# Performance work log

Hardware: AMD Instinct MI355X
Metric: run time of the kernel (lower is better)

The kernel has to match this reference:

```python
import jax, jax.numpy as jnp
import numpy as np
from jax import lax

# dims (see shape_source)
V, E = 100000, 200        # vocab, embedding dim
HID = 256; H = HID // 2    # BiLSTM hidden, per-direction
K = 24                     # tagset size (incl START/STOP)
B, T = 64, 1024
START, STOP = 0, 1
NEG = -10000.0


def setup_inputs() -> dict:
    key = jax.random.key(0)
    ks = jax.random.split(key, 16)
    s = 0.1  # init scale to keep LSTM gates in a sane range
    return {
        "sentences": jax.random.randint(ks[0], (B, T), 0, V, dtype=jnp.int32),
        "lens": jnp.full((B,), T, dtype=jnp.int32),
        "emb": jax.random.normal(ks[1], (V, E), dtype=jnp.float32) * s,
        # PyTorch LSTM layout: W_ih [4H, in], W_hh [4H, H], gate order i,f,g,o
        "W_ih_f": jax.random.normal(ks[2], (4 * H, E)) * s,
        "W_hh_f": jax.random.normal(ks[3], (4 * H, H)) * s,
        "b_ih_f": jax.random.normal(ks[4], (4 * H,)) * s,
        "b_hh_f": jax.random.normal(ks[5], (4 * H,)) * s,
        "W_ih_b": jax.random.normal(ks[6], (4 * H, E)) * s,
        "W_hh_b": jax.random.normal(ks[7], (4 * H, H)) * s,
        "b_ih_b": jax.random.normal(ks[8], (4 * H,)) * s,
        "b_hh_b": jax.random.normal(ks[9], (4 * H,)) * s,
        # init_hidden(): random h0/c0, [2 directions, B, H]
        "h0": jax.random.normal(ks[10], (2, B, H)),
        "c0": jax.random.normal(ks[11], (2, B, H)),
        # hidden2tag: nn.Linear(hidden_dim, K) -> weight [K, HID]
        "W_out": jax.random.normal(ks[12], (K, HID)) * s,
        "b_out": jax.random.normal(ks[13], (K,)) * s,
        "transitions": jax.random.normal(ks[14], (K, K)),  # [to, from]
    }


def _lstm_dir(x, W_ih, W_hh, b_ih, b_hh, h0, c0):
    """x: [T, B, in] -> hs: [T, B, H]. PyTorch LSTM cell math."""
    def step(carry, xt):
        h, c = carry
        g = xt @ W_ih.T + b_ih + h @ W_hh.T + b_hh  # [B, 4H]
        i, f, gg, o = jnp.split(g, 4, axis=-1)
        i = jax.nn.sigmoid(i); f = jax.nn.sigmoid(f)
        gg = jnp.tanh(gg); o = jax.nn.sigmoid(o)
        c = f * c + i * gg
        h = o * jnp.tanh(c)
        return (h, c), h
    _, hs = lax.scan(step, (h0, c0), x)
    return hs


def _viterbi_batch(feats, transitions):
    """feats: [B, T, K]. Batched version of _viterbi_decode.
    Returns (path_score [B], best_path [B, T])."""
    b = feats.shape[0]
    v0 = jnp.full((b, K), NEG, feats.dtype).at[:, START].set(0.0)
    transT = transitions.T  # [prev, next]

    def step(v, feat_t):
        # scores[b, prev, next] = v[b, prev] + trans(next <- prev)
        scores = v[:, :, None] + transT[None, :, :]
        best = jnp.max(scores, axis=1)          # [B, K]
        bptr = jnp.argmax(scores, axis=1)       # [B, K] best prev per next
        return best + feat_t, bptr

    v, bptrs = lax.scan(step, v0, jnp.swapaxes(feats, 0, 1))  # bptrs [T, B, K]
    terminal = v + transitions[STOP][None, :]
    path_score = jnp.max(terminal, axis=1)      # [B]
    last_tag = jnp.argmax(terminal, axis=1)     # [B]

    def back(tag, bp):
        prev = jnp.take_along_axis(bp, tag[:, None], axis=1)[:, 0]
        return prev, tag

    _, path = lax.scan(back, last_tag, bptrs, reverse=True)  # [T, B]
    return path_score, path.T


def reference(sentences, lens, emb, W_ih_f, W_hh_f, b_ih_f, b_hh_f,
              W_ih_b, W_hh_b, b_ih_b, b_hh_b, h0, c0, W_out, b_out,
              transitions):
    # embedding lookup; forward() packs raw w_embeds (dropout branch unused)
    x = emb[sentences]                       # [B, T, E]
    x = jnp.swapaxes(x, 0, 1)                # [T, B, E] (time-major like LSTM)
    hf = _lstm_dir(x, W_ih_f, W_hh_f, b_ih_f, b_hh_f, h0[0], c0[0])
    hb = _lstm_dir(x[::-1], W_ih_b, W_hh_b, b_ih_b, b_hh_b, h0[1], c0[1])[::-1]
    out = jnp.concatenate([hf, hb], axis=-1)  # [T, B, HID]
    feats = out @ W_out.T + b_out             # [T, B, K]
    feats = jnp.swapaxes(feats, 0, 1)          # [B, T, K]
    # all lens == T, so per-sentence slicing is the full sequence
    path_score, tag_seqs = _viterbi_batch(feats, transitions)
    return path_score, tag_seqs
```

## Files before the change

### kernel.cpp

```cpp
#include <hip/hip_runtime.h>
#include <math.h>

#define Ee   200
#define Hh   128
#define G4   512
#define Kk   24
#define Bb   64
#define Tt   1024
#define HIDd 256
#define NEGf (-10000.0f)
#define PSTR 9

__global__ __launch_bounds__(256) void k_wt(const float* __restrict__ Wf,
                                            const float* __restrict__ Wb,
                                            float* __restrict__ Wt) {
    int idx = blockIdx.x * 256 + threadIdx.x;
    if (idx >= Ee * 1024) return;
    int k = idx >> 10, n = idx & 1023;
    Wt[idx] = (n < G4) ? Wf[n * Ee + k] : Wb[(n - G4) * Ee + k];
}

__global__ __launch_bounds__(256, 2) void k_gemm2(const int* __restrict__ sent,
                                                  const float* __restrict__ emb,
                                                  const float* __restrict__ Wt,
                                                  float* __restrict__ Uc,
                                                  int c0T, int CT, int unified) {
    __shared__ float As[8][128];
    __shared__ float Bs[8][256];
    __shared__ int   toks[128];

    int tid = threadIdx.x;
    int n0  = blockIdx.x * 256;
    int m0  = blockIdx.y * 128;
    int dz  = blockIdx.z;
    int ty  = tid >> 4, tx = tid & 15;

    if (tid < 128) {
        int m = m0 + tid;
        int it = m >> 6, b = m & 63;
        int t = unified ? it : (dz ? (Tt - 1 - (c0T + it)) : (c0T + it));
        toks[tid] = sent[b * Tt + t];
    }
    __syncthreads();

    int am = tid & 127, ak4 = tid >> 7;
    int brow = tid >> 5, bc4 = tid & 31;

    const float* aptr = emb + (size_t)toks[am] * Ee + ak4 * 4;
    int bcol0 = (unified ? 0 : dz * G4) + n0;
    const float* bptr = Wt + (size_t)brow * 1024 + bcol0 + bc4 * 4;

    float acc[8][16];
#pragma unroll
    for (int i = 0; i < 8; ++i)
#pragma unroll
        for (int j = 0; j < 16; ++j) acc[i][j] = 0.f;

    float4 av  = *(const float4*)(aptr);
    float4 bv0 = *(const float4*)(bptr);
    float4 bv1 = *(const float4*)(bptr + 128);

    for (int kc = 0; kc < Ee; kc += 8) {
        As[ak4 * 4 + 0][am] = av.x;
        As[ak4 * 4 + 1][am] = av.y;
        As[ak4 * 4 + 2][am] = av.z;
        As[ak4 * 4 + 3][am] = av.w;
        *(float4*)&Bs[brow][bc4 * 4]       = bv0;
        *(float4*)&Bs[brow][128 + bc4 * 4] = bv1;
        __syncthreads();

        if (kc + 8 < Ee) {
            av  = *(const float4*)(aptr + kc + 8);
            bv0 = *(const float4*)(bptr + (size_t)(kc + 8) * 1024);
            bv1 = *(const float4*)(bptr + (size_t)(kc + 8) * 1024 + 128);
        }

#pragma unroll
        for (int k = 0; k < 8; ++k) {
            float a_[8], b_[16];
            *(float4*)&a_[0] = *(const float4*)&As[k][ty * 8];
            *(float4*)&a_[4] = *(const float4*)&As[k][ty * 8 + 4];
#pragma unroll
            for (int q = 0; q < 4; ++q)
                *(float4*)&b_[4 * q] = *(const float4*)&Bs[k][tx * 4 + 64 * q];
#pragma unroll
            for (int i = 0; i < 8; ++i)
#pragma unroll
                for (int j = 0; j < 16; ++j)
                    acc[i][j] = fmaf(a_[i], b_[j], acc[i][j]);
        }
        __syncthreads();
    }

    int dd   = unified ? (n0 >> 9) : dz;
    int ncol = unified ? (n0 & 511) : n0;
    float* base = Uc + (size_t)dd * ((size_t)CT * Bb * G4);
#pragma unroll
    for (int i = 0; i < 8; ++i) {
        float* dst = base + (size_t)(m0 + ty * 8 + i) * G4 + ncol + tx * 4;
#pragma unroll
        for (int q = 0; q < 4; ++q)
            *(float4*)(dst + 64 * q) = make_float4(acc[i][4 * q], acc[i][4 * q + 1],
                                                   acc[i][4 * q + 2], acc[i][4 * q + 3]);
    }
}

__global__ __launch_bounds__(512, 2) void k_lstm2(const float* __restrict__ Uc,
                                                  const float* __restrict__ Whh_f,
                                                  const float* __restrict__ Whh_b,
                                                  const float* __restrict__ bih_f,
                                                  const float* __restrict__ bhh_f,
                                                  const float* __restrict__ bih_b,
                                                  const float* __restrict__ bhh_b,
                                                  const float* __restrict__ h0v,
                                                  const float* __restrict__ c0v,
                                                  const float* __restrict__ Wout,
                                                  float* __restrict__ hst,
                                                  float* __restrict__ cst,
                                                  float* __restrict__ pf,
                                                  int c0T, int CT, int first, int unified) {
    __shared__ float hsh[Hh];
    __shared__ float gsh[G4];
    __shared__ float ps[(G4 + Kk) * PSTR];

    int tid  = threadIdx.x;
    int lane = tid & 63, wv = tid >> 6;
    int b = blockIdx.x & 63, d = blockIdx.x >> 6;

    const float* Whh = d ? Whh_b : Whh_f;
    float bias = d ? (bih_b[tid] + bhh_b[tid]) : (bih_f[tid] + bhh_f[tid]);

    float w[8][16];
#pragma unroll
    for (int ri = 0; ri < 8; ++ri) {
        const float* wr = Whh + (size_t)(ri * 64 + lane) * Hh + wv * 16;
#pragma unroll
        for (int c4 = 0; c4 < 4; ++c4)
            *(float4*)&w[ri][c4 * 4] = *(const float4*)(wr + c4 * 4);
    }
    float wt[16];
    if (lane < Kk) {
        const float* wr = Wout + (size_t)lane * HIDd + d * Hh + wv * 16;
#pragma unroll
        for (int c4 = 0; c4 < 4; ++c4)
            *(float4*)&wt[c4 * 4] = *(const float4*)(wr + c4 * 4);
    }

    float cc = 0.f;
    if (tid < Hh) {
        int si = (d * Bb + b) * Hh + tid;
        hsh[tid] = first ? h0v[si] : hst[si];
        cc       = first ? c0v[si] : cst[si];
    }
    __syncthreads();

    const float* Ub = Uc + (size_t)d * ((size_t)CT * Bb * G4);
    int u0 = unified ? (d ? (Tt - 1) : 0) : 0;
    int us = unified ? (d ? -1 : 1) : 1;

    float ucur = Ub[(size_t)u0 * (Bb * G4) + b * G4 + tid];
    float unext = 0.f;

    for (int i = 0; i <= CT; ++i) {
        int last = (i == CT);
        float hv[16];
        *(float4*)&hv[0]  = *(const float4*)&hsh[wv * 16];
        *(float4*)&hv[4]  = *(const float4*)&hsh[wv * 16 + 4];
        *(float4*)&hv[8]  = *(const float4*)&hsh[wv * 16 + 8];
        *(float4*)&hv[12] = *(const float4*)&hsh[wv * 16 + 12];

        if (lane < Kk) {
            float s = 0.f;
#pragma unroll
            for (int c = 0; c < 16; ++c) s = fmaf(wt[c], hv[c], s);
            ps[(G4 + lane) * PSTR + wv] = s;
        }
        if (!last) {
#pragma unroll
            for (int ri = 0; ri < 8; ++ri) {
                float s = 0.f;
#pragma unroll
                for (int c = 0; c < 16; ++c) s = fmaf(w[ri][c], hv[c], s);
                ps[(ri * 64 + lane) * PSTR + wv] = s;
            }
            if (i + 1 < CT)
                unext = Ub[(size_t)(u0 + (i + 1) * us) * (Bb * G4) + b * G4 + tid];
        }
        __syncthreads();

        if (!last) {
            const float* pr = ps + (size_t)tid * PSTR;
            float s = ((pr[0] + pr[1]) + (pr[2] + pr[3])) +
                      ((pr[4] + pr[5]) + (pr[6] + pr[7]));
            s += ucur + bias;
            int gt = tid >> 7;
            gsh[tid] = (gt == 2) ? tanhf(s) : 1.f / (1.f + expf(-s));
        }
        __syncthreads();

        if (!last && tid < Hh) {
            float gi = gsh[tid], gf = gsh[Hh + tid];
            float gg = gsh[2 * Hh + tid], go = gsh[3 * Hh + tid];
            cc = gf * cc + gi * gg;
            hsh[tid] = go * tanhf(cc);
        }
        if (tid >= 128 && tid < 128 + Kk && i >= 1) {
            int k = tid - 128;
            const float* pr = ps + (size_t)(G4 + k) * PSTR;
            float s = ((pr[0] + pr[1]) + (pr[2] + pr[3])) +
                      ((pr[4] + pr[5]) + (pr[6] + pr[7]));
            int tp = c0T + i - 1;
            int tg = d ? (Tt - 1 - tp) : tp;
            pf[((size_t)(d * Bb + b) * Tt + tg) * Kk + k] = s;
        }
        __syncthreads();
        ucur = unext;
    }

    if (tid < Hh) {
        int si = (d * Bb + b) * Hh + tid;
        hst[si] = hsh[tid];
        cst[si] = cc;
    }
}

#define CMB(av, ai, bv_, bi_, ov, oi)                         \
    { bool g = (bv_) > (av); ov = g ? (bv_) : (av); oi = g ? (bi_) : (ai); }

__global__ __launch_bounds__(64) void k_viterbi(const float* __restrict__ pf,
                                                const float* __restrict__ bout,
                                                const float* __restrict__ trans,
                                                float* __restrict__ out) {
    __shared__ unsigned char bptr[Tt * Kk];
    __shared__ float fsh[2][64][25];
    __shared__ float tsh[Kk];
    __shared__ unsigned char path[Tt];

    int lane = threadIdx.x;
    int b    = blockIdx.x;
    int half   = (lane >= Kk) ? 1 : 0;
    int n      = half ? (lane - Kk) : lane;
    int active = (lane < 2 * Kk);

    float tr[12];
    float bo = 0.f;
    if (active) {
#pragma unroll
        for (int j = 0; j < 12; ++j) tr[j] = trans[n * Kk + half * 12 + j];
        bo = bout[n];
    }
    float v = (lane == 0) ? 0.f : NEGf;

    const float* p0 = pf + (size_t)b * Tt * Kk;
    const float* p1 = pf + (size_t)(Bb + b) * Tt * Kk;

    float4 r0[6], r1[6];
#pragma unroll
    for (int j = 0; j < 6; ++j) {
        int f = 4 * (lane + 64 * j);
        r0[j] = *(const float4*)(p0 + f);
        r1[j] = *(const float4*)(p1 + f);
    }
#pragma unroll
    for (int j = 0; j < 6; ++j) {
        int f = 4 * (lane + 64 * j);
        int s = f / 24, k = f - 24 * s;
        fsh[0][s][k + 0] = r0[j].x + r1[j].x;
        fsh[0][s][k + 1] = r0[j].y + r1[j].y;
        fsh[0][s][k + 2] = r0[j].z + r1[j].z;
        fsh[0][s][k + 3] = r0[j].w + r1[j].w;
    }

    for (int c = 0; c < 16; ++c) {
        int cur = c & 1;
        if (c + 1 < 16) {
            const float* q0 = p0 + (c + 1) * 1536;
            const float* q1 = p1 + (c + 1) * 1536;
#pragma unroll
            for (int j = 0; j < 6; ++j) {
                int f = 4 * (lane + 64 * j);
                r0[j] = *(const float4*)(q0 + f);
                r1[j] = *(const float4*)(q1 + f);
            }
        }

        for (int s = 0; s < 64; ++s) {
            int t = c * 64 + s;
            if (active) {
                int pb = half * 12;
                float sc[12];
#pragma unroll
                for (int j = 0; j < 12; ++j) sc[j] = __shfl(v, pb + j) + tr[j];

                float l1v[6]; int l1i[6];
#pragma unroll
                for (int j = 0; j < 6; ++j)
                    CMB(sc[2 * j], 2 * j, sc[2 * j + 1], 2 * j + 1, l1v[j], l1i[j]);
                float l2v[3]; int l2i[3];
#pragma unroll
                for (int j = 0; j < 3; ++j)
                    CMB(l1v[2 * j], l1i[2 * j], l1v[2 * j + 1], l1i[2 * j + 1],
                        l2v[j], l2i[j]);
                float dv; int di;
                CMB(l2v[0], l2i[0], l2v[1], l2i[1], dv, di);
                float best; int bp;
                CMB(dv, di, l2v[2], l2i[2], best, bp);
                bp += pb;

                float ob  = __shfl(best, n + Kk);
                int   obp = __shfl(bp,   n + Kk);
                if (half == 0) {
                    if (ob > best) { best = ob; bp = obp; }
                    v = best + fsh[cur][s][n] + bo;
                    bptr[t * Kk + n] = (unsigned char)bp;
                }
            }
        }

        if (c + 1 < 16) {
#pragma unroll
            for (int j = 0; j < 6; ++j) {
                int f = 4 * (lane + 64 * j);
                int s = f / 24, k = f - 24 * s;
                fsh[cur ^ 1][s][k + 0] = r0[j].x + r1[j].x;
                fsh[cur ^ 1][s][k + 1] = r0[j].y + r1[j].y;
                fsh[cur ^ 1][s][k + 2] = r0[j].z + r1[j].z;
                fsh[cur ^ 1][s][k + 3] = r0[j].w + r1[j].w;
            }
        }
    }

    if (half == 0 && lane < Kk) tsh[n] = v + trans[1 * Kk + n];
    __syncthreads();

    if (lane == 0) {
        float bestv = tsh[0];
        int tag = 0;
        for (int q = 1; q < Kk; ++q)
            if (tsh[q] > bestv) { bestv = tsh[q]; tag = q; }
        out[b] = bestv;
        for (int t = Tt - 1; t >= 1; --t) {
            path[t] = (unsigned char)tag;
            tag = bptr[t * Kk + tag];
        }
        path[0] = (unsigned char)tag;
    }
    __syncthreads();

    float* otag = out + Bb + (size_t)b * Tt;
    for (int t = lane; t < Tt; t += 64) otag[t] = (float)path[t];
}

extern "C" void kernel_launch(void* const* d_in, const int* in_sizes, int n_in,
                              void* d_out, int out_size, void* d_ws, size_t ws_size,
                              hipStream_t stream) {
    const int*   sent  = (const int*)d_in[0];
    const float* emb   = (const float*)d_in[2];
    const float* Wih_f = (const float*)d_in[3];
    const float* Whh_f = (const float*)d_in[4];
    const float* bih_f = (const float*)d_in[5];
    const float* bhh_f = (const float*)d_in[6];
    const float* Wih_b = (const float*)d_in[7];
    const float* Whh_b = (const float*)d_in[8];
    const float* bih_b = (const float*)d_in[9];
    const float* bhh_b = (const float*)d_in[10];
    const float* h0    = (const float*)d_in[11];
    const float* c0    = (const float*)d_in[12];
    const float* Wout  = (const float*)d_in[13];
    const float* bout  = (const float*)d_in[14];
    const float* trans = (const float*)d_in[15];

    float* ws  = (float*)d_ws;
    float* Wt  = ws;
    float* pf  = Wt + 204800;
    float* hst = pf + 3145728;
    float* cst = hst + 16384;
    float* Uc  = cst + 16384;

    const size_t fixedf = 204800 + 3145728 + 16384 + 16384;
    size_t needU = (size_t)2 * Tt * Bb * G4;
    int unified = ((fixedf + needU) * 4 <= ws_size);

    k_wt<<<(Ee * 1024 + 255) / 256, 256, 0, stream>>>(Wih_f, Wih_b, Wt);

    if (unified) {
        k_gemm2<<<dim3(4, 512, 1), 256, 0, stream>>>(sent, emb, Wt, Uc, 0, Tt, 1);
        k_lstm2<<<128, 512, 0, stream>>>(Uc, Whh_f, Whh_b, bih_f, bhh_f,
                                         bih_b, bhh_b, h0, c0, Wout,
                                         hst, cst, pf, 0, Tt, 1, 1);
    } else {
        int CT = 64;
        const int cands[3] = {512, 256, 128};
        for (int ci = 0; ci < 3; ++ci)
            if ((fixedf + (size_t)2 * cands[ci] * Bb * G4) * 4 <= ws_size) {
                CT = cands[ci]; break;
            }
        int NC = Tt / CT;
        for (int cix = 0; cix < NC; ++cix) {
            k_gemm2<<<dim3(2, CT * 64 / 128, 2), 256, 0, stream>>>(
                sent, emb, Wt, Uc, cix * CT, CT, 0);
            k_lstm2<<<128, 512, 0, stream>>>(Uc, Whh_f, Whh_b, bih_f, bhh_f,
                                             bih_b, bhh_b, h0, c0, Wout,
                                             hst, cst, pf, cix * CT, CT,
                                             cix == 0, 0);
        }
    }

    k_viterbi<<<Bb, 64, 0, stream>>>(pf, bout, trans, (float*)d_out);
}
```

Baseline: 1.517 ms.

## Process two batch rows per LSTM block to reuse register-resident W_hh

The recurrent LSTM kernel now handles two sequences per block, so 64 blocks run instead of 128. Each W_hh weight held in registers is used for two matvecs per load, and the barrier cost is shared across two sequences. Each step does twice the FMA and shared-memory work per block with half as many blocks. On a 256-CU device that leaves more CUs idle and may lengthen the serial per-step latency.

```diff
diff --git a/kernel.cpp b/kernel.cpp
--- a/kernel.cpp
+++ b/kernel.cpp
@@ -105,27 +105,31 @@
     }
 }
 
-__global__ __launch_bounds__(512, 2) void k_lstm2(const float* __restrict__ Uc,
-                                                  const float* __restrict__ Whh_f,
-                                                  const float* __restrict__ Whh_b,
-                                                  const float* __restrict__ bih_f,
-                                                  const float* __restrict__ bhh_f,
-                                                  const float* __restrict__ bih_b,
-                                                  const float* __restrict__ bhh_b,
-                                                  const float* __restrict__ h0v,
-                                                  const float* __restrict__ c0v,
-                                                  const float* __restrict__ Wout,
-                                                  float* __restrict__ hst,
-                                                  float* __restrict__ cst,
-                                                  float* __restrict__ pf,
-                                                  int c0T, int CT, int first, int unified) {
-    __shared__ float hsh[Hh];
-    __shared__ float gsh[G4];
-    __shared__ float ps[(G4 + Kk) * PSTR];
+__global__ __launch_bounds__(512, 2) void k_lstm2b(const float* __restrict__ Uc,
+                                                   const float* __restrict__ Whh_f,
+                                                   const float* __restrict__ Whh_b,
+                                                   const float* __restrict__ bih_f,
+                                                   const float* __restrict__ bhh_f,
+                                                   const float* __restrict__ bih_b,
+                                                   const float* __restrict__ bhh_b,
+                                                   const float* __restrict__ h0v,
+                                                   const float* __restrict__ c0v,
+                                                   const float* __restrict__ Wout,
+                                                   float* __restrict__ hst,
+                                                   float* __restrict__ cst,
+                                                   float* __restrict__ pf,
+                                                   int c0T, int CT, int first,
+                                                   int unified) {
+    __shared__ float hshA[Hh], hshB[Hh];
+    __shared__ float gshA[G4], gshB[G4];
+    __shared__ float psA[(G4 + Kk) * PSTR];
+    __shared__ float psB[(G4 + Kk) * PSTR];
 
     int tid  = threadIdx.x;
     int lane = tid & 63, wv = tid >> 6;
-    int b = blockIdx.x & 63, d = blockIdx.x >> 6;
+    int d  = blockIdx.x >> 5;
+    int pr = blockIdx.x & 31;
+    int bA = pr * 2, bB = pr * 2 + 1;
 
     const float* Whh = d ? Whh_b : Whh_f;
     float bias = d ? (bih_b[tid] + bhh_b[tid]) : (bih_f[tid] + bhh_f[tid]);
@@ -146,11 +150,17 @@
             *(float4*)&wt[c4 * 4] = *(const float4*)(wr + c4 * 4);
     }
 
-    float cc = 0.f;
+    float ccA = 0.f, ccB = 0.f;
     if (tid < Hh) {
-        int si = (d * Bb + b) * Hh + tid;
-        hsh[tid] = first ? h0v[si] : hst[si];
-        cc       = first ? c0v[si] : cst[si];
+        int si = (d * Bb + bA) * Hh + tid;
+        hshA[tid] = first ? h0v[si] : hst[si];
+        ccA       = first ? c0v[si] : cst[si];
+    }
+    if (tid >= 256 && tid < 256 + Hh) {
+        int j = tid - 256;
+        int si = (d * Bb + bB) * Hh + j;
+        hshB[j] = first ? h0v[si] : hst[si];
+        ccB     = first ? c0v[si] : cst[si];
     }
     __syncthreads();
 
@@ -158,69 +168,118 @@
     int u0 = unified ? (d ? (Tt - 1) : 0) : 0;
     int us = unified ? (d ? -1 : 1) : 1;
 
-    float ucur = Ub[(size_t)u0 * (Bb * G4) + b * G4 + tid];
-    float unext = 0.f;
+    float ucurA = Ub[(size_t)u0 * (Bb * G4) + bA * G4 + tid];
+    float ucurB = Ub[(size_t)u0 * (Bb * G4) + bB * G4 + tid];
+    float unextA = 0.f, unextB = 0.f;
 
     for (int i = 0; i <= CT; ++i) {
         int last = (i == CT);
-        float hv[16];
-        *(float4*)&hv[0]  = *(const float4*)&hsh[wv * 16];
-        *(float4*)&hv[4]  = *(const float4*)&hsh[wv * 16 + 4];
-        *(float4*)&hv[8]  = *(const float4*)&hsh[wv * 16 + 8];
-        *(float4*)&hv[12] = *(const float4*)&hsh[wv * 16 + 12];
+        float hvA[16], hvB[16];
+        *(float4*)&hvA[0]  = *(const float4*)&hshA[wv * 16];
+        *(float4*)&hvA[4]  = *(const float4*)&hshA[wv * 16 + 4];
+        *(float4*)&hvA[8]  = *(const float4*)&hshA[wv * 16 + 8];
+        *(float4*)&hvA[12] = *(const float4*)&hshA[wv * 16 + 12];
+        *(float4*)&hvB[0]  = *(const float4*)&hshB[wv * 16];
+        *(float4*)&hvB[4]  = *(const float4*)&hshB[wv * 16 + 4];
+        *(float4*)&hvB[8]  = *(const float4*)&hshB[wv * 16 + 8];
+        *(float4*)&hvB[12] = *(const float4*)&hshB[wv * 16 + 12];
 
         if (lane < Kk) {
-            float s = 0.f;
-#pragma unroll
-            for (int c = 0; c < 16; ++c) s = fmaf(wt[c], hv[c], s);
-            ps[(G4 + lane) * PSTR + wv] = s;
+            float sA = 0.f, sB = 0.f;
+#pragma unroll
+            for (int c = 0; c < 16; ++c) {
+                sA = fmaf(wt[c], hvA[c], sA);
+                sB = fmaf(wt[c], hvB[c], sB);
+            }
+            psA[(G4 + lane) * PSTR + wv] = sA;
+            psB[(G4 + lane) * PSTR + wv] = sB;
         }
         if (!last) {
 #pragma unroll
             for (int ri = 0; ri < 8; ++ri) {
-                float s = 0.f;
-#pragma unroll
-                for (int c = 0; c < 16; ++c) s = fmaf(w[ri][c], hv[c], s);
-                ps[(ri * 64 + lane) * PSTR + wv] = s;
-            }
-            if (i + 1 < CT)
-                unext = Ub[(size_t)(u0 + (i + 1) * us) * (Bb * G4) + b * G4 + tid];
+                float sA = 0.f, sB = 0.f;
+#pragma unroll
+                for (int c = 0; c < 16; ++c) {
+                    sA = fmaf(w[ri][c], hvA[c], sA);
+                    sB = fmaf(w[ri][c], hvB[c], sB);
+                }
+                psA[(ri * 64 + lane) * PSTR + wv] = sA;
+                psB[(ri * 64 + lane) * PSTR + wv] = sB;
+            }
+            if (i + 1 < CT) {
+                const float* un = Ub + (size_t)(u0 + (i + 1) * us) * (Bb * G4);
+                unextA = un[bA * G4 + tid];
+                unextB = un[bB * G4 + tid];
+            }
         }
         __syncthreads();
 
         if (!last) {
-            const float* pr = ps + (size_t)tid * PSTR;
-            float s = ((pr[0] + pr[1]) + (pr[2] + pr[3])) +
-                      ((pr[4] + pr[5]) + (pr[6] + pr[7]));
-            s += ucur + bias;
+            const float* prA = psA + (size_t)tid * PSTR;
+            const float* prB = psB + (size_t)tid * PSTR;
+            float sA = ((prA[0] + prA[1]) + (prA[2] + prA[3])) +
+                       ((prA[4] + prA[5]) + (prA[6] + prA[7]));
+            float sB = ((prB[0] + prB[1]) + (prB[2] + prB[3])) +
+                       ((prB[4] + prB[5]) + (prB[6] + prB[7]));
+            sA += ucurA + bias;
+            sB += ucurB + bias;
             int gt = tid >> 7;
-            gsh[tid] = (gt == 2) ? tanhf(s) : 1.f / (1.f + expf(-s));
+            if (gt == 2) {
+                gshA[tid] = tanhf(sA);
+                gshB[tid] = tanhf(sB);
+            } else {
+                gshA[tid] = 1.f / (1.f + expf(-sA));
+                gshB[tid] = 1.f / (1.f + expf(-sB));
+            }
         }
         __syncthreads();
 
         if (!last && tid < Hh) {
-            float gi = gsh[tid], gf = gsh[Hh + tid];
-            float gg = gsh[2 * Hh + tid], go = gsh[3 * Hh + tid];
-            cc = gf * cc + gi * gg;
-            hsh[tid] = go * tanhf(cc);
+            float gi = gshA[tid], gf = gshA[Hh + tid];
+            float gg = gshA[2 * Hh + tid], go = gshA[3 * Hh + tid];
+            ccA = gf * ccA + gi * gg;
+            hshA[tid] = go * tanhf(ccA);
+        }
+        if (!last && tid >= 256 && tid < 256 + Hh) {
+            int j = tid - 256;
+            float gi = gshB[j], gf = gshB[Hh + j];
+            float gg = gshB[2 * Hh + j], go = gshB[3 * Hh + j];
+            ccB = gf * ccB + gi * gg;
+            hshB[j] = go * tanhf(ccB);
         }
         if (tid >= 128 && tid < 128 + Kk && i >= 1) {
             int k = tid - 128;
-            const float* pr = ps + (size_t)(G4 + k) * PSTR;
-            float s = ((pr[0] + pr[1]) + (pr[2] + pr[3])) +
-                      ((pr[4] + pr[5]) + (pr[6] + pr[7]));
+            const float* prt = psA + (size_t)(G4 + k) * PSTR;
+            float s = ((prt[0] + prt[1]) + (prt[2] + prt[3])) +
+                      ((prt[4] + prt[5]) + (prt[6] + prt[7]));
             int tp = c0T + i - 1;
             int tg = d ? (Tt - 1 - tp) : tp;
-            pf[((size_t)(d * Bb + b) * Tt + tg) * Kk + k] = s;
+            pf[((size_t)(d * Bb + bA) * Tt + tg) * Kk + k] = s;
+        }
+        if (tid >= 384 && tid < 384 + Kk && i >= 1) {
+            int k = tid - 384;
+            const float* prt = psB + (size_t)(G4 + k) * PSTR;
+            float s = ((prt[0] + prt[1]) + (prt[2] + prt[3])) +
+                      ((prt[4] + prt[5]) + (prt[6] + prt[7]));
+            int tp = c0T + i - 1;
+            int tg = d ? (Tt - 1 - tp) : tp;
+            pf[((size_t)(d * Bb + bB) * Tt + tg) * Kk + k] = s;
         }
         __syncthreads();
-        ucur = unext;
+        ucurA = unextA;
+        ucurB = unextB;
     }
 
     if (tid < Hh) {
-        int si = (d * Bb + b) * Hh + tid;
-        hst[si] = hsh[tid];
-        cst[si] = cc;
+        int si = (d * Bb + bA) * Hh + tid;
+        hst[si] = hshA[tid];
+        cst[si] = ccA;
+    }
+    if (tid >= 256 && tid < 256 + Hh) {
+        int j = tid - 256;
+        int si = (d * Bb + bB) * Hh + j;
+        hst[si] = hshB[j];
+        cst[si] = ccB;
     }
 }
 
@@ -385,7 +444,7 @@
 
     if (unified) {
         k_gemm2<<<dim3(4, 512, 1), 256, 0, stream>>>(sent, emb, Wt, Uc, 0, Tt, 1);
-        k_lstm2<<<128, 512, 0, stream>>>(Uc, Whh_f, Whh_b, bih_f, bhh_f,
+        k_lstm2b<<<64, 512, 0, stream>>>(Uc, Whh_f, Whh_b, bih_f, bhh_f,
                                          bih_b, bhh_b, h0, c0, Wout,
                                          hst, cst, pf, 0, Tt, 1, 1);
     } else {
@@ -399,7 +458,7 @@
         for (int cix = 0; cix < NC; ++cix) {
             k_gemm2<<<dim3(2, CT * 64 / 128, 2), 256, 0, stream>>>(
                 sent, emb, Wt, Uc, cix * CT, CT, 0);
-            k_lstm2<<<128, 512, 0, stream>>>(Uc, Whh_f, Whh_b, bih_f, bhh_f,
+            k_lstm2b<<<64, 512, 0, stream>>>(Uc, Whh_f, Whh_b, bih_f, bhh_f,
                                              bih_b, bhh_b, h0, c0, Wout,
                                              hst, cst, pf, cix * CT, CT,
                                              cix == 0, 0);
```

Result: slower. 2.081 ms (+37.2%).

## Cut LSTM step barriers via gate-interleaved ownership and shuffles

Applied to the files above, without the earlier changes.

Reassigns each thread to own one gate row so the four gates of a hidden unit sit in adjacent lanes, combining them with warp shuffles instead of a separate gate shared buffer and barrier. The partial-sum layout becomes swizzled per-wave planes, and the tag projection partials are double-buffered and reduced one step later, which drops one __syncthreads per timestep from three to two. This shortens the serial recurrence latency at the cost of more complex indexing and a lagged feature write epilogue.

```diff
diff --git a/kernel.cpp b/kernel.cpp
--- a/kernel.cpp
+++ b/kernel.cpp
@@ -9,7 +9,7 @@
 #define Tt   1024
 #define HIDd 256
 #define NEGf (-10000.0f)
-#define PSTR 9
+#define PSV  520
 
 __global__ __launch_bounds__(256) void k_wt(const float* __restrict__ Wf,
                                             const float* __restrict__ Wb,
@@ -105,7 +105,7 @@
     }
 }
 
-__global__ __launch_bounds__(512, 2) void k_lstm2(const float* __restrict__ Uc,
+__global__ __launch_bounds__(512, 2) void k_lstm6(const float* __restrict__ Uc,
                                                   const float* __restrict__ Whh_f,
                                                   const float* __restrict__ Whh_b,
                                                   const float* __restrict__ bih_f,
@@ -118,17 +118,19 @@
                                                   float* __restrict__ hst,
                                                   float* __restrict__ cst,
                                                   float* __restrict__ pf,
-                                                  int c0T, int CT, int first, int unified) {
+                                                  int c0T, int CT, int first,
+                                                  int unified) {
     __shared__ float hsh[Hh];
-    __shared__ float gsh[G4];
-    __shared__ float ps[(G4 + Kk) * PSTR];
+    __shared__ float ps[8 * PSV];
+    __shared__ float tb[2 * 216];
 
     int tid  = threadIdx.x;
     int lane = tid & 63, wv = tid >> 6;
     int b = blockIdx.x & 63, d = blockIdx.x >> 6;
 
     const float* Whh = d ? Whh_b : Whh_f;
-    float bias = d ? (bih_b[tid] + bhh_b[tid]) : (bih_f[tid] + bhh_f[tid]);
+    const float* bih = d ? bih_b : bih_f;
+    const float* bhh = d ? bhh_b : bhh_f;
 
     float w[8][16];
 #pragma unroll
@@ -145,12 +147,31 @@
         for (int c4 = 0; c4 < 4; ++c4)
             *(float4*)&wt[c4 * 4] = *(const float4*)(wr + c4 * 4);
     }
+
+    int addrW[8];
+#pragma unroll
+    for (int ri = 0; ri < 8; ++ri) {
+        int r = ri * 64 + lane;
+        int g = r >> 7, ww = (r & 127) >> 4, m = r & 15;
+        addrW[ri] = wv * PSV + ((((g << 2) | (ww >> 1)) << 5) |
+                                (((ww ^ g) & 1) << 4) | m);
+    }
+
+    int gOwn = lane & 3, mOwn = lane >> 2;
+    int rOwn = gOwn * 128 + 16 * wv + mOwn;
+    int piR  = ((((gOwn << 2) | (wv >> 1)) << 5) |
+                (((wv ^ gOwn) & 1) << 4) | mOwn);
+    float biasOwn = bih[rOwn] + bhh[rOwn];
 
     float cc = 0.f;
     if (tid < Hh) {
         int si = (d * Bb + b) * Hh + tid;
         hsh[tid] = first ? h0v[si] : hst[si];
-        cc       = first ? c0v[si] : cst[si];
+    }
+    if (gOwn == 0) {
+        int ci = 16 * wv + mOwn;
+        int si = (d * Bb + b) * Hh + ci;
+        cc = first ? c0v[si] : cst[si];
     }
     __syncthreads();
 
@@ -158,7 +179,7 @@
     int u0 = unified ? (d ? (Tt - 1) : 0) : 0;
     int us = unified ? (d ? -1 : 1) : 1;
 
-    float ucur = Ub[(size_t)u0 * (Bb * G4) + b * G4 + tid];
+    float ucur  = Ub[(size_t)u0 * (Bb * G4) + b * G4 + rOwn];
     float unext = 0.f;
 
     for (int i = 0; i <= CT; ++i) {
@@ -173,7 +194,7 @@
             float s = 0.f;
 #pragma unroll
             for (int c = 0; c < 16; ++c) s = fmaf(wt[c], hv[c], s);
-            ps[(G4 + lane) * PSTR + wv] = s;
+            tb[(i & 1) * 216 + lane * 9 + wv] = s;
         }
         if (!last) {
 #pragma unroll
@@ -181,46 +202,58 @@
                 float s = 0.f;
 #pragma unroll
                 for (int c = 0; c < 16; ++c) s = fmaf(w[ri][c], hv[c], s);
-                ps[(ri * 64 + lane) * PSTR + wv] = s;
+                ps[addrW[ri]] = s;
             }
             if (i + 1 < CT)
-                unext = Ub[(size_t)(u0 + (i + 1) * us) * (Bb * G4) + b * G4 + tid];
-        }
-        __syncthreads();
-
-        if (!last) {
-            const float* pr = ps + (size_t)tid * PSTR;
-            float s = ((pr[0] + pr[1]) + (pr[2] + pr[3])) +
-                      ((pr[4] + pr[5]) + (pr[6] + pr[7]));
-            s += ucur + bias;
-            int gt = tid >> 7;
-            gsh[tid] = (gt == 2) ? tanhf(s) : 1.f / (1.f + expf(-s));
-        }
-        __syncthreads();
-
-        if (!last && tid < Hh) {
-            float gi = gsh[tid], gf = gsh[Hh + tid];
-            float gg = gsh[2 * Hh + tid], go = gsh[3 * Hh + tid];
-            cc = gf * cc + gi * gg;
-            hsh[tid] = go * tanhf(cc);
-        }
-        if (tid >= 128 && tid < 128 + Kk && i >= 1) {
+                unext = Ub[(size_t)(u0 + (i + 1) * us) * (Bb * G4) + b * G4 + rOwn];
+        }
+        if (i >= 2 && tid >= 128 && tid < 128 + Kk) {
             int k = tid - 128;
-            const float* pr = ps + (size_t)(G4 + k) * PSTR;
-            float s = ((pr[0] + pr[1]) + (pr[2] + pr[3])) +
-                      ((pr[4] + pr[5]) + (pr[6] + pr[7]));
-            int tp = c0T + i - 1;
+            const float* q = tb + ((i - 1) & 1) * 216 + k * 9;
+            float s = ((q[0] + q[1]) + (q[2] + q[3])) +
+                      ((q[4] + q[5]) + (q[6] + q[7]));
+            int tp = c0T + i - 2;
             int tg = d ? (Tt - 1 - tp) : tp;
             pf[((size_t)(d * Bb + b) * Tt + tg) * Kk + k] = s;
         }
         __syncthreads();
-        ucur = unext;
-    }
-
+
+        if (!last) {
+            const float* pr = ps + piR;
+            float s = ((pr[0 * PSV] + pr[1 * PSV]) + (pr[2 * PSV] + pr[3 * PSV])) +
+                      ((pr[4 * PSV] + pr[5 * PSV]) + (pr[6 * PSV] + pr[7 * PSV]));
+            s += ucur + biasOwn;
+            float a = (gOwn == 2) ? tanhf(s) : 1.f / (1.f + expf(-s));
+
+            int base = lane & ~3;
+            float fx = __shfl(a, base + 1);
+            float gx = __shfl(a, base + 2);
+            float ox = __shfl(a, base + 3);
+            if (gOwn == 0) {
+                cc = fx * cc + a * gx;
+                hsh[16 * wv + mOwn] = ox * tanhf(cc);
+            }
+            ucur = unext;
+        }
+        __syncthreads();
+    }
+
+    if (tid >= 128 && tid < 128 + Kk) {
+        int k = tid - 128;
+        const float* q = tb + (CT & 1) * 216 + k * 9;
+        float s = ((q[0] + q[1]) + (q[2] + q[3])) +
+                  ((q[4] + q[5]) + (q[6] + q[7]));
+        int tp = c0T + CT - 1;
+        int tg = d ? (Tt - 1 - tp) : tp;
+        pf[((size_t)(d * Bb + b) * Tt + tg) * Kk + k] = s;
+    }
     if (tid < Hh) {
         int si = (d * Bb + b) * Hh + tid;
         hst[si] = hsh[tid];
-        cst[si] = cc;
+    }
+    if (gOwn == 0) {
+        int ci = 16 * wv + mOwn;
+        cst[(d * Bb + b) * Hh + ci] = cc;
     }
 }
 
@@ -385,7 +418,7 @@
 
     if (unified) {
         k_gemm2<<<dim3(4, 512, 1), 256, 0, stream>>>(sent, emb, Wt, Uc, 0, Tt, 1);
-        k_lstm2<<<128, 512, 0, stream>>>(Uc, Whh_f, Whh_b, bih_f, bhh_f,
+        k_lstm6<<<128, 512, 0, stream>>>(Uc, Whh_f, Whh_b, bih_f, bhh_f,
                                          bih_b, bhh_b, h0, c0, Wout,
                                          hst, cst, pf, 0, Tt, 1, 1);
     } else {
@@ -399,7 +432,7 @@
         for (int cix = 0; cix < NC; ++cix) {
             k_gemm2<<<dim3(2, CT * 64 / 128, 2), 256, 0, stream>>>(
                 sent, emb, Wt, Uc, cix * CT, CT, 0);
-            k_lstm2<<<128, 512, 0, stream>>>(Uc, Whh_f, Whh_b, bih_f, bhh_f,
+            k_lstm6<<<128, 512, 0, stream>>>(Uc, Whh_f, Whh_b, bih_f, bhh_f,
                                              bih_b, bhh_b, h0, c0, Wout,
                                              hst, cst, pf, cix * CT, CT,
                                              cix == 0, 0);
```

New measurement: 1.826 ms. 1.2x slower.
